# Kernel tuning notes

Measured on AMD Instinct MI355X. Metric: run time of the kernel, lower is better.

The kernel has to match this reference:

```python
import jax, jax.numpy as jnp
import numpy as np

H = 128  # hidden size
I = 19   # input size


def _uniform(key, shape, bound):
    return jax.random.uniform(key, shape, dtype=jnp.float32, minval=-bound, maxval=bound)


def setup_inputs() -> dict:
    key = jax.random.key(0)
    ks = jax.random.split(key, 9)
    bound = 1.0 / np.sqrt(H)  # torch nn.RNN init: U(-1/sqrt(H), 1/sqrt(H))
    x = jax.random.normal(ks[0], (256, 1024, I), dtype=jnp.float32)
    return {
        "x": x,
        "W_ih0": _uniform(ks[1], (H, I), bound),
        "W_hh0": _uniform(ks[2], (H, H), bound),
        "b_ih0": _uniform(ks[3], (H,), bound),
        "b_hh0": _uniform(ks[4], (H,), bound),
        "W_ih1": _uniform(ks[5], (H, H), bound),
        "W_hh1": _uniform(ks[6], (H, H), bound),
        "b_ih1": _uniform(ks[7], (H,), bound),
        "b_hh1": _uniform(ks[8], (H,), bound),
    }


def _rnn_layer(inp, W_ih, W_hh, b_ih, b_hh):
    # inp: [B, T, F]. Precompute input projection for all timesteps (one big GEMM),
    # then scan only the recurrent part: h_t = tanh(pre_t + h_{t-1} @ W_hh^T).
    pre = jnp.einsum('btf,hf->bth', inp, W_ih) + b_ih + b_hh  # [B, T, H]
    h0 = jnp.zeros((inp.shape[0], H), dtype=inp.dtype)

    def step(h, p_t):
        h = jnp.tanh(p_t + h @ W_hh.T)
        return h, h

    _, ys = jax.lax.scan(step, h0, jnp.swapaxes(pre, 0, 1))  # ys: [T, B, H]
    return jnp.swapaxes(ys, 0, 1)  # [B, T, H]


def reference(x, W_ih0, W_hh0, b_ih0, b_hh0, W_ih1, W_hh1, b_ih1, b_hh1):
    out1 = _rnn_layer(x, W_ih0, W_hh0, b_ih0, b_hh0)
    out2 = _rnn_layer(out1, W_ih1, W_hh1, b_ih1, b_hh1)
    return out2
```

## Files before the change

kernel.cpp:

```cpp
#include <hip/hip_runtime.h>
#include <math.h>

#define BATCH 256
#define T 1024
#define IN 19
#define H 128

__device__ __forceinline__ float fast_tanh(float x) {
    float ax = fabsf(x);
    float e  = __expf(2.0f * ax);
    float r  = 1.0f - 2.0f / (e + 1.0f);
    return copysignf(r, x);
}

template <int CTRL>
__device__ __forceinline__ float dppf(float v) {
    return __int_as_float(__builtin_amdgcn_update_dpp(
        0, __float_as_int(v), CTRL, 0xF, 0xF, true));
}
#define XOR1 0xB1
#define XOR2 0x4E
#define XOR8 0x128

__device__ __forceinline__ int uoff(int u) { return (u >> 4) * 20 + (u & 15); }

__global__ __launch_bounds__(512, 2)
void fused_rnn(const float* __restrict__ x,
               const float* __restrict__ Wih0,
               const float* __restrict__ Whh0,
               const float* __restrict__ bih0,
               const float* __restrict__ bhh0,
               const float* __restrict__ Wih1,
               const float* __restrict__ Whh1,
               const float* __restrict__ bih1,
               const float* __restrict__ bhh1,
               float* __restrict__ out) {
    const int b   = blockIdx.x;
    const int tid = threadIdx.x;

    __shared__ __align__(16) float h0ring[4][160];
    __shared__ __align__(16) float h1ring[4][160];
    __shared__ __align__(16) float Bring[4][H];
    __shared__ __align__(16) float xbuf[2][8 * 20];

    if (tid < 128) {
        __builtin_amdgcn_s_setprio(1);
        const bool b0 = tid & 1, b1 = tid & 2, b2 = tid & 8;
        const int s    = (tid & 3) | ((tid & 8) >> 1);
        const int G    = (tid >> 4) * 2 + ((tid >> 2) & 1);
        const int ub   = G * 8;
        const int ufin = ub + (b0 ? 4 : 0) + (b1 ? 2 : 0) + (b2 ? 1 : 0);

        float wA[8][16];
#pragma unroll
        for (int u = 0; u < 8; ++u) {
            const float* wr = Whh0 + (size_t)(ub + u) * H + s * 16;
#pragma unroll
            for (int c = 0; c < 16; c += 4) {
                float4 v = *(const float4*)&wr[c];
                wA[u][c] = v.x; wA[u][c+1] = v.y; wA[u][c+2] = v.z; wA[u][c+3] = v.w;
            }
        }
        float wI[20];
#pragma unroll
        for (int f = 0; f < IN; ++f) wI[f] = Wih0[ufin * IN + f];
        wI[19] = 0.0f;
        const float bias0 = bih0[ufin] + bhh0[ufin];

        const float* xsrc = x + (size_t)b * T * IN;
        const int idx0  = tid;
        const int idx1  = tid + 128;
        const bool v1   = (idx1 < 8 * IN);
        const int slot0 = (idx0 / IN) * 20 + idx0 % IN;
        const int slot1 = (idx1 / IN) * 20 + idx1 % IN;

        if (tid < 8) { xbuf[0][tid * 20 + 19] = 0.0f; xbuf[1][tid * 20 + 19] = 0.0f; }
        xbuf[0][slot0] = xsrc[idx0];
        if (v1) xbuf[0][slot1] = xsrc[idx1];
        float xr0 = xsrc[8 * IN + idx0];
        float xr1 = v1 ? xsrc[8 * IN + idx1] : 0.0f;

        h0ring[3][uoff(ufin)] = 0.0f;
        __syncthreads();

        const int so = s * 20;
        const int wo = uoff(ufin);
        for (int ko = 0; ko < T; ko += 8) {
            const int cb = (ko >> 3) & 1;
            const float* xch = xbuf[cb];
#pragma unroll
            for (int j = 0; j < 8; ++j) {
                const float* xp = &xch[j * 20];
                float4 xv0 = *(const float4*)&xp[0];
                float4 xv1 = *(const float4*)&xp[4];
                float4 xv2 = *(const float4*)&xp[8];
                float4 xv3 = *(const float4*)&xp[12];
                float4 xv4 = *(const float4*)&xp[16];
                float p0 = bias0, p1 = 0.0f;
                p0 = fmaf(xv0.x, wI[0],  p0); p1 = fmaf(xv0.y, wI[1],  p1);
                p0 = fmaf(xv0.z, wI[2],  p0); p1 = fmaf(xv0.w, wI[3],  p1);
                p0 = fmaf(xv1.x, wI[4],  p0); p1 = fmaf(xv1.y, wI[5],  p1);
                p0 = fmaf(xv1.z, wI[6],  p0); p1 = fmaf(xv1.w, wI[7],  p1);
                p0 = fmaf(xv2.x, wI[8],  p0); p1 = fmaf(xv2.y, wI[9],  p1);
                p0 = fmaf(xv2.z, wI[10], p0); p1 = fmaf(xv2.w, wI[11], p1);
                p0 = fmaf(xv3.x, wI[12], p0); p1 = fmaf(xv3.y, wI[13], p1);
                p0 = fmaf(xv3.z, wI[14], p0); p1 = fmaf(xv3.w, wI[15], p1);
                p0 = fmaf(xv4.x, wI[16], p0); p1 = fmaf(xv4.y, wI[17], p1);
                p0 = fmaf(xv4.z, wI[18], p0); p1 = fmaf(xv4.w, wI[19], p1);
                const float* hp = &h0ring[(j + 3) & 3][so];
                float d0=0,d1=0,d2=0,d3=0,d4=0,d5=0,d6=0,d7=0;
#pragma unroll
                for (int c = 0; c < 16; c += 4) {
                    float4 hv = *(const float4*)&hp[c];
                    d0 = fmaf(wA[0][c],hv.x,d0); d0 = fmaf(wA[0][c+1],hv.y,d0); d0 = fmaf(wA[0][c+2],hv.z,d0); d0 = fmaf(wA[0][c+3],hv.w,d0);
                    d1 = fmaf(wA[1][c],hv.x,d1); d1 = fmaf(wA[1][c+1],hv.y,d1); d1 = fmaf(wA[1][c+2],hv.z,d1); d1 = fmaf(wA[1][c+3],hv.w,d1);
                    d2 = fmaf(wA[2][c],hv.x,d2); d2 = fmaf(wA[2][c+1],hv.y,d2); d2 = fmaf(wA[2][c+2],hv.z,d2); d2 = fmaf(wA[2][c+3],hv.w,d2);
                    d3 = fmaf(wA[3][c],hv.x,d3); d3 = fmaf(wA[3][c+1],hv.y,d3); d3 = fmaf(wA[3][c+2],hv.z,d3); d3 = fmaf(wA[3][c+3],hv.w,d3);
                    d4 = fmaf(wA[4][c],hv.x,d4); d4 = fmaf(wA[4][c+1],hv.y,d4); d4 = fmaf(wA[4][c+2],hv.z,d4); d4 = fmaf(wA[4][c+3],hv.w,d4);
                    d5 = fmaf(wA[5][c],hv.x,d5); d5 = fmaf(wA[5][c+1],hv.y,d5); d5 = fmaf(wA[5][c+2],hv.z,d5); d5 = fmaf(wA[5][c+3],hv.w,d5);
                    d6 = fmaf(wA[6][c],hv.x,d6); d6 = fmaf(wA[6][c+1],hv.y,d6); d6 = fmaf(wA[6][c+2],hv.z,d6); d6 = fmaf(wA[6][c+3],hv.w,d6);
                    d7 = fmaf(wA[7][c],hv.x,d7); d7 = fmaf(wA[7][c+1],hv.y,d7); d7 = fmaf(wA[7][c+2],hv.z,d7); d7 = fmaf(wA[7][c+3],hv.w,d7);
                }
                float e0 = (b0 ? d4 : d0) + dppf<XOR1>(b0 ? d0 : d4);
                float e1 = (b0 ? d5 : d1) + dppf<XOR1>(b0 ? d1 : d5);
                float e2 = (b0 ? d6 : d2) + dppf<XOR1>(b0 ? d2 : d6);
                float e3 = (b0 ? d7 : d3) + dppf<XOR1>(b0 ? d3 : d7);
                float g0 = (b1 ? e2 : e0) + dppf<XOR2>(b1 ? e0 : e2);
                float g1 = (b1 ? e3 : e1) + dppf<XOR2>(b1 ? e1 : e3);
                float f  = (b2 ? g1 : g0) + dppf<XOR8>(b2 ? g0 : g1);
                h0ring[j & 3][wo] = fast_tanh(f + p0 + p1);
                if (j == 7) {
                    if (ko + 8 < T) {
                        float* xd = xbuf[cb ^ 1];
                        xd[slot0] = xr0;
                        if (v1) xd[slot1] = xr1;
                    }
                    if (ko + 16 < T) {
                        const float* xs2 = xsrc + (size_t)(ko + 16) * IN;
                        xr0 = xs2[idx0];
                        if (v1) xr1 = xs2[idx1];
                    }
                }
                __syncthreads();
            }
        }
        __syncthreads();
        __syncthreads();
    } else if (tid < 384) {
        const int p  = tid - 128;
        const bool b0 = p & 1, b1 = p & 2;
        const int s    = (p & 3) | ((p & 8) >> 1);
        const int Gp   = (p >> 4) * 2 + ((p >> 2) & 1);
        const int ub   = Gp * 4;
        const int ufin = ub + (b0 ? 2 : 0) + (b1 ? 1 : 0);

        float wP[4][16];
#pragma unroll
        for (int u = 0; u < 4; ++u) {
            const float* wr = Wih1 + (size_t)(ub + u) * H + s * 16;
#pragma unroll
            for (int c = 0; c < 16; c += 4) {
                float4 v = *(const float4*)&wr[c];
                wP[u][c] = v.x; wP[u][c+1] = v.y; wP[u][c+2] = v.z; wP[u][c+3] = v.w;
            }
        }
        const float biasP = bih1[ufin] + bhh1[ufin];

        __syncthreads();
        __syncthreads();

        const int so = s * 20;
        for (int ko = 1; ko < 1025; ko += 8) {
#pragma unroll
            for (int j = 0; j < 8; ++j) {
                const float* hp = &h0ring[j & 3][so];
                float d0=0,d1=0,d2=0,d3=0;
#pragma unroll
                for (int c = 0; c < 16; c += 4) {
                    float4 hv = *(const float4*)&hp[c];
                    d0 = fmaf(wP[0][c],hv.x,d0); d0 = fmaf(wP[0][c+1],hv.y,d0); d0 = fmaf(wP[0][c+2],hv.z,d0); d0 = fmaf(wP[0][c+3],hv.w,d0);
                    d1 = fmaf(wP[1][c],hv.x,d1); d1 = fmaf(wP[1][c+1],hv.y,d1); d1 = fmaf(wP[1][c+2],hv.z,d1); d1 = fmaf(wP[1][c+3],hv.w,d1);
                    d2 = fmaf(wP[2][c],hv.x,d2); d2 = fmaf(wP[2][c+1],hv.y,d2); d2 = fmaf(wP[2][c+2],hv.z,d2); d2 = fmaf(wP[2][c+3],hv.w,d2);
                    d3 = fmaf(wP[3][c],hv.x,d3); d3 = fmaf(wP[3][c+1],hv.y,d3); d3 = fmaf(wP[3][c+2],hv.z,d3); d3 = fmaf(wP[3][c+3],hv.w,d3);
                }
                float e0 = (b0 ? d2 : d0) + dppf<XOR1>(b0 ? d0 : d2);
                float e1 = (b0 ? d3 : d1) + dppf<XOR1>(b0 ? d1 : d3);
                float g  = (b1 ? e1 : e0) + dppf<XOR2>(b1 ? e0 : e1);
                g += dppf<XOR8>(g);
                if (!(p & 8)) Bring[j & 3][ufin] = g + biasP;
                __syncthreads();
            }
        }
        __syncthreads();
    } else {
        __builtin_amdgcn_s_setprio(1);
        const int w  = tid - 384;
        const bool b0 = w & 1, b1 = w & 2, b2 = w & 8;
        const int s    = (w & 3) | ((w & 8) >> 1);
        const int G    = (w >> 4) * 2 + ((w >> 2) & 1);
        const int ub   = G * 8;
        const int ufin = ub + (b0 ? 4 : 0) + (b1 ? 2 : 0) + (b2 ? 1 : 0);

        float wA[8][16];
#pragma unroll
        for (int u = 0; u < 8; ++u) {
            const float* wr = Whh1 + (size_t)(ub + u) * H + s * 16;
#pragma unroll
            for (int c = 0; c < 16; c += 4) {
                float4 v = *(const float4*)&wr[c];
                wA[u][c] = v.x; wA[u][c+1] = v.y; wA[u][c+2] = v.z; wA[u][c+3] = v.w;
            }
        }
        float* orow = out + (size_t)b * T * H + ufin;
        float sbuf[8];

        h1ring[3][uoff(ufin)] = 0.0f;
        __syncthreads();
        __syncthreads();
        __syncthreads();

        const int so = s * 20;
        const int wo = uoff(ufin);
        for (int ko = 2; ko < 1026; ko += 8) {
#pragma unroll
            for (int j = 0; j < 8; ++j) {
                const float* hp = &h1ring[(j + 3) & 3][so];
                float Bg = Bring[j & 3][ufin];
                float d0=0,d1=0,d2=0,d3=0,d4=0,d5=0,d6=0,d7=0;
#pragma unroll
                for (int c = 0; c < 16; c += 4) {
                    float4 hv = *(const float4*)&hp[c];
                    d0 = fmaf(wA[0][c],hv.x,d0); d0 = fmaf(wA[0][c+1],hv.y,d0); d0 = fmaf(wA[0][c+2],hv.z,d0); d0 = fmaf(wA[0][c+3],hv.w,d0);
                    d1 = fmaf(wA[1][c],hv.x,d1); d1 = fmaf(wA[1][c+1],hv.y,d1); d1 = fmaf(wA[1][c+2],hv.z,d1); d1 = fmaf(wA[1][c+3],hv.w,d1);
                    d2 = fmaf(wA[2][c],hv.x,d2); d2 = fmaf(wA[2][c+1],hv.y,d2); d2 = fmaf(wA[2][c+2],hv.z,d2); d2 = fmaf(wA[2][c+3],hv.w,d2);
                    d3 = fmaf(wA[3][c],hv.x,d3); d3 = fmaf(wA[3][c+1],hv.y,d3); d3 = fmaf(wA[3][c+2],hv.z,d3); d3 = fmaf(wA[3][c+3],hv.w,d3);
                    d4 = fmaf(wA[4][c],hv.x,d4); d4 = fmaf(wA[4][c+1],hv.y,d4); d4 = fmaf(wA[4][c+2],hv.z,d4); d4 = fmaf(wA[4][c+3],hv.w,d4);
                    d5 = fmaf(wA[5][c],hv.x,d5); d5 = fmaf(wA[5][c+1],hv.y,d5); d5 = fmaf(wA[5][c+2],hv.z,d5); d5 = fmaf(wA[5][c+3],hv.w,d5);
                    d6 = fmaf(wA[6][c],hv.x,d6); d6 = fmaf(wA[6][c+1],hv.y,d6); d6 = fmaf(wA[6][c+2],hv.z,d6); d6 = fmaf(wA[6][c+3],hv.w,d6);
                    d7 = fmaf(wA[7][c],hv.x,d7); d7 = fmaf(wA[7][c+1],hv.y,d7); d7 = fmaf(wA[7][c+2],hv.z,d7); d7 = fmaf(wA[7][c+3],hv.w,d7);
                }
                float e0 = (b0 ? d4 : d0) + dppf<XOR1>(b0 ? d0 : d4);
                float e1 = (b0 ? d5 : d1) + dppf<XOR1>(b0 ? d1 : d5);
                float e2 = (b0 ? d6 : d2) + dppf<XOR1>(b0 ? d2 : d6);
                float e3 = (b0 ? d7 : d3) + dppf<XOR1>(b0 ? d3 : d7);
                float g0 = (b1 ? e2 : e0) + dppf<XOR2>(b1 ? e0 : e2);
                float g1 = (b1 ? e3 : e1) + dppf<XOR2>(b1 ? e1 : e3);
                float f  = (b2 ? g1 : g0) + dppf<XOR8>(b2 ? g0 : g1);
                float h1v = fast_tanh(Bg + f);
                h1ring[j & 3][wo] = h1v;
                sbuf[j] = h1v;
                if (j == 7) {
                    const int t0 = ko - 2;
#pragma unroll
                    for (int i = 0; i < 8; ++i)
                        orow[(size_t)(t0 + i) * H] = sbuf[i];
                }
                __syncthreads();
            }
        }
    }
}

extern "C" void kernel_launch(void* const* d_in, const int* in_sizes, int n_in,
                              void* d_out, int out_size, void* d_ws, size_t ws_size,
                              hipStream_t stream) {
    const float* x     = (const float*)d_in[0];
    const float* W_ih0 = (const float*)d_in[1];
    const float* W_hh0 = (const float*)d_in[2];
    const float* b_ih0 = (const float*)d_in[3];
    const float* b_hh0 = (const float*)d_in[4];
    const float* W_ih1 = (const float*)d_in[5];
    const float* W_hh1 = (const float*)d_in[6];
    const float* b_ih1 = (const float*)d_in[7];
    const float* b_hh1 = (const float*)d_in[8];

    float* out = (float*)d_out;

    fused_rnn<<<BATCH, 512, 0, stream>>>(x, W_ih0, W_hh0, b_ih0, b_hh0,
                                         W_ih1, W_hh1, b_ih1, b_hh1, out);
}
```

Baseline: 658.7 us.

## Move layer-0 input projection to middle warps and use lightweight barriers

The layer-0 input projection and x staging move out of the critical recurrent warp into the layer-1 projection warps. Those warps compute the next timestep's projection into a new shared ring buffer one step ahead, and the layer-1 pipeline stage is shifted to match. All __syncthreads calls are replaced with a custom barrier that waits only on LDS counters, not global memory. This shortens the serial layer-0 step, at the cost of more work on the middle warps and subtler memory-ordering assumptions around the barrier.

```diff
diff --git a/kernel.cpp b/kernel.cpp
--- a/kernel.cpp
+++ b/kernel.cpp
@@ -21,6 +21,12 @@
 #define XOR1 0xB1
 #define XOR2 0x4E
 #define XOR8 0x128
+
+__device__ __forceinline__ void sync_fast() {
+    asm volatile("s_waitcnt lgkmcnt(0)" ::: "memory");
+    __builtin_amdgcn_s_barrier();
+    asm volatile("" ::: "memory");
+}
 
 __device__ __forceinline__ int uoff(int u) { return (u >> 4) * 20 + (u & 15); }
 
@@ -41,6 +47,7 @@
     __shared__ __align__(16) float h0ring[4][160];
     __shared__ __align__(16) float h1ring[4][160];
     __shared__ __align__(16) float Bring[4][H];
+    __shared__ __align__(16) float projring[4][H];
     __shared__ __align__(16) float xbuf[2][8 * 20];
 
     if (tid < 128) {
@@ -61,53 +68,24 @@
                 wA[u][c] = v.x; wA[u][c+1] = v.y; wA[u][c+2] = v.z; wA[u][c+3] = v.w;
             }
         }
-        float wI[20];
-#pragma unroll
-        for (int f = 0; f < IN; ++f) wI[f] = Wih0[ufin * IN + f];
-        wI[19] = 0.0f;
-        const float bias0 = bih0[ufin] + bhh0[ufin];
-
-        const float* xsrc = x + (size_t)b * T * IN;
-        const int idx0  = tid;
-        const int idx1  = tid + 128;
-        const bool v1   = (idx1 < 8 * IN);
-        const int slot0 = (idx0 / IN) * 20 + idx0 % IN;
-        const int slot1 = (idx1 / IN) * 20 + idx1 % IN;
-
-        if (tid < 8) { xbuf[0][tid * 20 + 19] = 0.0f; xbuf[1][tid * 20 + 19] = 0.0f; }
-        xbuf[0][slot0] = xsrc[idx0];
-        if (v1) xbuf[0][slot1] = xsrc[idx1];
-        float xr0 = xsrc[8 * IN + idx0];
-        float xr1 = v1 ? xsrc[8 * IN + idx1] : 0.0f;
-
+        {
+            const float* wr = Wih0 + ufin * IN;
+            const float* xr = x + (size_t)b * T * IN;
+            float acc = bih0[ufin] + bhh0[ufin];
+#pragma unroll
+            for (int f = 0; f < IN; ++f) acc = fmaf(xr[f], wr[f], acc);
+            projring[0][ufin] = acc;
+        }
         h0ring[3][uoff(ufin)] = 0.0f;
-        __syncthreads();
+        sync_fast();
 
         const int so = s * 20;
         const int wo = uoff(ufin);
         for (int ko = 0; ko < T; ko += 8) {
-            const int cb = (ko >> 3) & 1;
-            const float* xch = xbuf[cb];
 #pragma unroll
             for (int j = 0; j < 8; ++j) {
-                const float* xp = &xch[j * 20];
-                float4 xv0 = *(const float4*)&xp[0];
-                float4 xv1 = *(const float4*)&xp[4];
-                float4 xv2 = *(const float4*)&xp[8];
-                float4 xv3 = *(const float4*)&xp[12];
-                float4 xv4 = *(const float4*)&xp[16];
-                float p0 = bias0, p1 = 0.0f;
-                p0 = fmaf(xv0.x, wI[0],  p0); p1 = fmaf(xv0.y, wI[1],  p1);
-                p0 = fmaf(xv0.z, wI[2],  p0); p1 = fmaf(xv0.w, wI[3],  p1);
-                p0 = fmaf(xv1.x, wI[4],  p0); p1 = fmaf(xv1.y, wI[5],  p1);
-                p0 = fmaf(xv1.z, wI[6],  p0); p1 = fmaf(xv1.w, wI[7],  p1);
-                p0 = fmaf(xv2.x, wI[8],  p0); p1 = fmaf(xv2.y, wI[9],  p1);
-                p0 = fmaf(xv2.z, wI[10], p0); p1 = fmaf(xv2.w, wI[11], p1);
-                p0 = fmaf(xv3.x, wI[12], p0); p1 = fmaf(xv3.y, wI[13], p1);
-                p0 = fmaf(xv3.z, wI[14], p0); p1 = fmaf(xv3.w, wI[15], p1);
-                p0 = fmaf(xv4.x, wI[16], p0); p1 = fmaf(xv4.y, wI[17], p1);
-                p0 = fmaf(xv4.z, wI[18], p0); p1 = fmaf(xv4.w, wI[19], p1);
                 const float* hp = &h0ring[(j + 3) & 3][so];
+                float pcur = projring[j & 3][ufin];
                 float d0=0,d1=0,d2=0,d3=0,d4=0,d5=0,d6=0,d7=0;
 #pragma unroll
                 for (int c = 0; c < 16; c += 4) {
@@ -128,24 +106,12 @@
                 float g0 = (b1 ? e2 : e0) + dppf<XOR2>(b1 ? e0 : e2);
                 float g1 = (b1 ? e3 : e1) + dppf<XOR2>(b1 ? e1 : e3);
                 float f  = (b2 ? g1 : g0) + dppf<XOR8>(b2 ? g0 : g1);
-                h0ring[j & 3][wo] = fast_tanh(f + p0 + p1);
-                if (j == 7) {
-                    if (ko + 8 < T) {
-                        float* xd = xbuf[cb ^ 1];
-                        xd[slot0] = xr0;
-                        if (v1) xd[slot1] = xr1;
-                    }
-                    if (ko + 16 < T) {
-                        const float* xs2 = xsrc + (size_t)(ko + 16) * IN;
-                        xr0 = xs2[idx0];
-                        if (v1) xr1 = xs2[idx1];
-                    }
-                }
-                __syncthreads();
-            }
-        }
-        __syncthreads();
-        __syncthreads();
+                h0ring[j & 3][wo] = fast_tanh(pcur + f);
+                sync_fast();
+            }
+        }
+        sync_fast();
+        sync_fast();
     } else if (tid < 384) {
         const int p  = tid - 128;
         const bool b0 = p & 1, b1 = p & 2;
@@ -166,14 +132,39 @@
         }
         const float biasP = bih1[ufin] + bhh1[ufin];
 
-        __syncthreads();
-        __syncthreads();
+        const bool hasProj = (p >= 128);
+        const int pu = p - 128;
+        float wIP[20];
+        float biasPr = 0.0f;
+        const float* xsrc = x + (size_t)b * T * IN + IN;
+        const int idx0  = pu;
+        const int idx1  = pu + 128;
+        const bool v1   = hasProj && (pu < 24);
+        const int slot0 = hasProj ? ((idx0 / IN) * 20 + idx0 % IN) : 0;
+        const int slot1 = hasProj ? ((idx1 / IN) * 20 + idx1 % IN) : 0;
+        const int XMAX  = (T - 1) * IN - 1;
+        float xr0 = 0.0f, xr1 = 0.0f;
+
+        if (hasProj) {
+            const float* wr = Wih0 + (size_t)pu * IN;
+#pragma unroll
+            for (int f = 0; f < IN; ++f) wIP[f] = wr[f];
+            wIP[19] = 0.0f;
+            biasPr = bih0[pu] + bhh0[pu];
+            if (pu < 8) { xbuf[0][pu * 20 + 19] = 0.0f; xbuf[1][pu * 20 + 19] = 0.0f; }
+            xbuf[0][slot0] = xsrc[idx0];
+            if (v1) xbuf[0][slot1] = xsrc[idx1];
+            xr0 = xsrc[152 + idx0];
+            if (v1) xr1 = xsrc[152 + idx1];
+        }
+        sync_fast();
 
         const int so = s * 20;
-        for (int ko = 1; ko < 1025; ko += 8) {
+        for (int ko = 0; ko < T; ko += 8) {
+            const int cb = (ko >> 3) & 1;
 #pragma unroll
             for (int j = 0; j < 8; ++j) {
-                const float* hp = &h0ring[j & 3][so];
+                const float* hp = &h0ring[(j + 3) & 3][so];
                 float d0=0,d1=0,d2=0,d3=0;
 #pragma unroll
                 for (int c = 0; c < 16; c += 4) {
@@ -187,11 +178,59 @@
                 float e1 = (b0 ? d3 : d1) + dppf<XOR1>(b0 ? d1 : d3);
                 float g  = (b1 ? e1 : e0) + dppf<XOR2>(b1 ? e0 : e1);
                 g += dppf<XOR8>(g);
-                if (!(p & 8)) Bring[j & 3][ufin] = g + biasP;
-                __syncthreads();
-            }
-        }
-        __syncthreads();
+                if (!(p & 8)) Bring[(j + 3) & 3][ufin] = g + biasP;
+                if (hasProj) {
+                    const float* xp = &xbuf[cb][j * 20];
+                    float4 xv0 = *(const float4*)&xp[0];
+                    float4 xv1 = *(const float4*)&xp[4];
+                    float4 xv2 = *(const float4*)&xp[8];
+                    float4 xv3 = *(const float4*)&xp[12];
+                    float4 xv4 = *(const float4*)&xp[16];
+                    float p0 = biasPr, p1 = 0.0f;
+                    p0 = fmaf(xv0.x, wIP[0],  p0); p1 = fmaf(xv0.y, wIP[1],  p1);
+                    p0 = fmaf(xv0.z, wIP[2],  p0); p1 = fmaf(xv0.w, wIP[3],  p1);
+                    p0 = fmaf(xv1.x, wIP[4],  p0); p1 = fmaf(xv1.y, wIP[5],  p1);
+                    p0 = fmaf(xv1.z, wIP[6],  p0); p1 = fmaf(xv1.w, wIP[7],  p1);
+                    p0 = fmaf(xv2.x, wIP[8],  p0); p1 = fmaf(xv2.y, wIP[9],  p1);
+                    p0 = fmaf(xv2.z, wIP[10], p0); p1 = fmaf(xv2.w, wIP[11], p1);
+                    p0 = fmaf(xv3.x, wIP[12], p0); p1 = fmaf(xv3.y, wIP[13], p1);
+                    p0 = fmaf(xv3.z, wIP[14], p0); p1 = fmaf(xv3.w, wIP[15], p1);
+                    p0 = fmaf(xv4.x, wIP[16], p0); p1 = fmaf(xv4.y, wIP[17], p1);
+                    p0 = fmaf(xv4.z, wIP[18], p0); p1 = fmaf(xv4.w, wIP[19], p1);
+                    projring[(j + 1) & 3][pu] = p0 + p1;
+                    if (j == 7) {
+                        float* xd = xbuf[cb ^ 1];
+                        xd[slot0] = xr0;
+                        if (v1) xd[slot1] = xr1;
+                        const int c2 = (ko >> 3) + 2;
+                        int o0 = 152 * c2 + idx0; o0 = o0 > XMAX ? XMAX : o0;
+                        int o1 = 152 * c2 + idx1; o1 = o1 > XMAX ? XMAX : o1;
+                        xr0 = xsrc[o0];
+                        if (v1) xr1 = xsrc[o1];
+                    }
+                }
+                sync_fast();
+            }
+        }
+        {
+            const float* hp = &h0ring[3][so];
+            float d0=0,d1=0,d2=0,d3=0;
+#pragma unroll
+            for (int c = 0; c < 16; c += 4) {
+                float4 hv = *(const float4*)&hp[c];
+                d0 = fmaf(wP[0][c],hv.x,d0); d0 = fmaf(wP[0][c+1],hv.y,d0); d0 = fmaf(wP[0][c+2],hv.z,d0); d0 = fmaf(wP[0][c+3],hv.w,d0);
+                d1 = fmaf(wP[1][c],hv.x,d1); d1 = fmaf(wP[1][c+1],hv.y,d1); d1 = fmaf(wP[1][c+2],hv.z,d1); d1 = fmaf(wP[1][c+3],hv.w,d1);
+                d2 = fmaf(wP[2][c],hv.x,d2); d2 = fmaf(wP[2][c+1],hv.y,d2); d2 = fmaf(wP[2][c+2],hv.z,d2); d2 = fmaf(wP[2][c+3],hv.w,d2);
+                d3 = fmaf(wP[3][c],hv.x,d3); d3 = fmaf(wP[3][c+1],hv.y,d3); d3 = fmaf(wP[3][c+2],hv.z,d3); d3 = fmaf(wP[3][c+3],hv.w,d3);
+            }
+            float e0 = (b0 ? d2 : d0) + dppf<XOR1>(b0 ? d0 : d2);
+            float e1 = (b0 ? d3 : d1) + dppf<XOR1>(b0 ? d1 : d3);
+            float g  = (b1 ? e1 : e0) + dppf<XOR2>(b1 ? e0 : e1);
+            g += dppf<XOR8>(g);
+            if (!(p & 8)) Bring[3][ufin] = g + biasP;
+        }
+        sync_fast();
+        sync_fast();
     } else {
         __builtin_amdgcn_s_setprio(1);
         const int w  = tid - 384;
@@ -215,9 +254,9 @@
         float sbuf[8];
 
         h1ring[3][uoff(ufin)] = 0.0f;
-        __syncthreads();
-        __syncthreads();
-        __syncthreads();
+        sync_fast();
+        sync_fast();
+        sync_fast();
 
         const int so = s * 20;
         const int wo = uoff(ufin);
@@ -255,7 +294,7 @@
                     for (int i = 0; i < 8; ++i)
                         orow[(size_t)(t0 + i) * H] = sbuf[i];
                 }
-                __syncthreads();
+                sync_fast();
             }
         }
     }
```

Result: faster. 608.7 us (-7.6%).

## Replace block barriers with per-wave LDS flag dataflow pipeline across RNN stages

Applied to the files above, without the earlier changes.

Replaces the per-timestep __syncthreads lockstep with per-wave progress counters in shared memory that each stage spins on, so layer-0 recurrence, layer-1 input projection, layer-0 input projection and layer-1 recurrence can run decoupled through 8-deep ring buffers. The layer-0 input projection moves from the recurrence waves into a dedicated pair of waves, which removes it from the critical serial path. The layer-1 projection is rebalanced to 8 units per thread. Spin-waiting with s_sleep and waitcnt fences adds polling cost and relies on LDS ordering between waves, and a spin cap could silently break correctness if a wait ever exceeds it.

```diff
diff --git a/kernel.cpp b/kernel.cpp
--- a/kernel.cpp
+++ b/kernel.cpp
@@ -22,9 +22,14 @@
 #define XOR2 0x4E
 #define XOR8 0x128
 
+#define FENCE asm volatile("" ::: "memory")
+#define LGKM0 asm volatile("s_waitcnt lgkmcnt(0)" ::: "memory")
+#define MAXSPIN (1 << 22)
+
 __device__ __forceinline__ int uoff(int u) { return (u >> 4) * 20 + (u & 15); }
 
-__global__ __launch_bounds__(512, 2)
+__global__ __launch_bounds__(512)
+__attribute__((amdgpu_waves_per_eu(2, 2)))
 void fused_rnn(const float* __restrict__ x,
                const float* __restrict__ Wih0,
                const float* __restrict__ Whh0,
@@ -38,18 +43,30 @@
     const int b   = blockIdx.x;
     const int tid = threadIdx.x;
 
-    __shared__ __align__(16) float h0ring[4][160];
-    __shared__ __align__(16) float h1ring[4][160];
-    __shared__ __align__(16) float Bring[4][H];
-    __shared__ __align__(16) float xbuf[2][8 * 20];
-
+    __shared__ __align__(16) float h0ring[8][160];
+    __shared__ __align__(16) float h1ring[8][160];
+    __shared__ __align__(16) float Bring[8][H];
+    __shared__ __align__(16) float projring[8][H];
+    __shared__ __align__(8)  int  flags[8];
+    volatile int* vf = (volatile int*)flags;
+
+    if (tid < 8) flags[tid] = 0;
     if (tid < 128) {
+        h0ring[7][uoff(tid)] = 0.0f;
+        h1ring[7][uoff(tid)] = 0.0f;
+    }
+    __syncthreads();
+
+    const int wave = tid >> 6;
+
+    if (wave < 2) {
         __builtin_amdgcn_s_setprio(1);
         const bool b0 = tid & 1, b1 = tid & 2, b2 = tid & 8;
         const int s    = (tid & 3) | ((tid & 8) >> 1);
         const int G    = (tid >> 4) * 2 + ((tid >> 2) & 1);
         const int ub   = G * 8;
         const int ufin = ub + (b0 ? 4 : 0) + (b1 ? 2 : 0) + (b2 ? 1 : 0);
+        const int myf  = wave;
 
         float wA[8][16];
 #pragma unroll
@@ -61,53 +78,26 @@
                 wA[u][c] = v.x; wA[u][c+1] = v.y; wA[u][c+2] = v.z; wA[u][c+3] = v.w;
             }
         }
-        float wI[20];
-#pragma unroll
-        for (int f = 0; f < IN; ++f) wI[f] = Wih0[ufin * IN + f];
-        wI[19] = 0.0f;
-        const float bias0 = bih0[ufin] + bhh0[ufin];
-
-        const float* xsrc = x + (size_t)b * T * IN;
-        const int idx0  = tid;
-        const int idx1  = tid + 128;
-        const bool v1   = (idx1 < 8 * IN);
-        const int slot0 = (idx0 / IN) * 20 + idx0 % IN;
-        const int slot1 = (idx1 / IN) * 20 + idx1 % IN;
-
-        if (tid < 8) { xbuf[0][tid * 20 + 19] = 0.0f; xbuf[1][tid * 20 + 19] = 0.0f; }
-        xbuf[0][slot0] = xsrc[idx0];
-        if (v1) xbuf[0][slot1] = xsrc[idx1];
-        float xr0 = xsrc[8 * IN + idx0];
-        float xr1 = v1 ? xsrc[8 * IN + idx1] : 0.0f;
-
-        h0ring[3][uoff(ufin)] = 0.0f;
-        __syncthreads();
-
         const int so = s * 20;
         const int wo = uoff(ufin);
+
         for (int ko = 0; ko < T; ko += 8) {
-            const int cb = (ko >> 3) & 1;
-            const float* xch = xbuf[cb];
 #pragma unroll
             for (int j = 0; j < 8; ++j) {
-                const float* xp = &xch[j * 20];
-                float4 xv0 = *(const float4*)&xp[0];
-                float4 xv1 = *(const float4*)&xp[4];
-                float4 xv2 = *(const float4*)&xp[8];
-                float4 xv3 = *(const float4*)&xp[12];
-                float4 xv4 = *(const float4*)&xp[16];
-                float p0 = bias0, p1 = 0.0f;
-                p0 = fmaf(xv0.x, wI[0],  p0); p1 = fmaf(xv0.y, wI[1],  p1);
-                p0 = fmaf(xv0.z, wI[2],  p0); p1 = fmaf(xv0.w, wI[3],  p1);
-                p0 = fmaf(xv1.x, wI[4],  p0); p1 = fmaf(xv1.y, wI[5],  p1);
-                p0 = fmaf(xv1.z, wI[6],  p0); p1 = fmaf(xv1.w, wI[7],  p1);
-                p0 = fmaf(xv2.x, wI[8],  p0); p1 = fmaf(xv2.y, wI[9],  p1);
-                p0 = fmaf(xv2.z, wI[10], p0); p1 = fmaf(xv2.w, wI[11], p1);
-                p0 = fmaf(xv3.x, wI[12], p0); p1 = fmaf(xv3.y, wI[13], p1);
-                p0 = fmaf(xv3.z, wI[14], p0); p1 = fmaf(xv3.w, wI[15], p1);
-                p0 = fmaf(xv4.x, wI[16], p0); p1 = fmaf(xv4.y, wI[17], p1);
-                p0 = fmaf(xv4.z, wI[18], p0); p1 = fmaf(xv4.w, wI[19], p1);
-                const float* hp = &h0ring[(j + 3) & 3][so];
+                const int k = ko + j;
+                {
+                    const int np = k + 1, nh = k, nb = k - 7;
+                    for (int it = 0; ; ++it) {
+                        if (vf[4] >= np && vf[5] >= np &&
+                            vf[0] >= nh && vf[1] >= nh &&
+                            vf[2] >= nb && vf[3] >= nb) break;
+                        if (it >= MAXSPIN) break;
+                        __builtin_amdgcn_s_sleep(1);
+                    }
+                    FENCE;
+                }
+                float pcur = projring[j][ufin];
+                const float* hp = &h0ring[(j + 7) & 7][so];
                 float d0=0,d1=0,d2=0,d3=0,d4=0,d5=0,d6=0,d7=0;
 #pragma unroll
                 for (int c = 0; c < 16; c += 4) {
@@ -128,78 +118,120 @@
                 float g0 = (b1 ? e2 : e0) + dppf<XOR2>(b1 ? e0 : e2);
                 float g1 = (b1 ? e3 : e1) + dppf<XOR2>(b1 ? e1 : e3);
                 float f  = (b2 ? g1 : g0) + dppf<XOR8>(b2 ? g0 : g1);
-                h0ring[j & 3][wo] = fast_tanh(f + p0 + p1);
-                if (j == 7) {
-                    if (ko + 8 < T) {
-                        float* xd = xbuf[cb ^ 1];
-                        xd[slot0] = xr0;
-                        if (v1) xd[slot1] = xr1;
-                    }
-                    if (ko + 16 < T) {
-                        const float* xs2 = xsrc + (size_t)(ko + 16) * IN;
-                        xr0 = xs2[idx0];
-                        if (v1) xr1 = xs2[idx1];
-                    }
-                }
-                __syncthreads();
-            }
-        }
-        __syncthreads();
-        __syncthreads();
-    } else if (tid < 384) {
+                h0ring[j][wo] = fast_tanh(pcur + f);
+                LGKM0;
+                vf[myf] = k + 1;
+                FENCE;
+            }
+        }
+    } else if (wave < 4) {
         const int p  = tid - 128;
-        const bool b0 = p & 1, b1 = p & 2;
+        const bool b0 = p & 1, b1 = p & 2, b2 = p & 8;
         const int s    = (p & 3) | ((p & 8) >> 1);
-        const int Gp   = (p >> 4) * 2 + ((p >> 2) & 1);
-        const int ub   = Gp * 4;
-        const int ufin = ub + (b0 ? 2 : 0) + (b1 ? 1 : 0);
-
-        float wP[4][16];
-#pragma unroll
-        for (int u = 0; u < 4; ++u) {
+        const int G    = (p >> 4) * 2 + ((p >> 2) & 1);
+        const int ub   = G * 8;
+        const int ufin = ub + (b0 ? 4 : 0) + (b1 ? 2 : 0) + (b2 ? 1 : 0);
+        const int myf  = 2 + (wave - 2);
+
+        float wB[8][16];
+#pragma unroll
+        for (int u = 0; u < 8; ++u) {
             const float* wr = Wih1 + (size_t)(ub + u) * H + s * 16;
 #pragma unroll
             for (int c = 0; c < 16; c += 4) {
                 float4 v = *(const float4*)&wr[c];
-                wP[u][c] = v.x; wP[u][c+1] = v.y; wP[u][c+2] = v.z; wP[u][c+3] = v.w;
+                wB[u][c] = v.x; wB[u][c+1] = v.y; wB[u][c+2] = v.z; wB[u][c+3] = v.w;
             }
         }
         const float biasP = bih1[ufin] + bhh1[ufin];
-
-        __syncthreads();
-        __syncthreads();
-
         const int so = s * 20;
-        for (int ko = 1; ko < 1025; ko += 8) {
+
+        for (int ko = 0; ko < T; ko += 8) {
 #pragma unroll
             for (int j = 0; j < 8; ++j) {
-                const float* hp = &h0ring[j & 3][so];
-                float d0=0,d1=0,d2=0,d3=0;
+                const int k = ko + j;
+                {
+                    const int nh = k + 1, nl = k - 7;
+                    for (int it = 0; ; ++it) {
+                        if (vf[0] >= nh && vf[1] >= nh &&
+                            vf[6] >= nl && vf[7] >= nl) break;
+                        if (it >= MAXSPIN) break;
+                        __builtin_amdgcn_s_sleep(1);
+                    }
+                    FENCE;
+                }
+                const float* hp = &h0ring[j][so];
+                float d0=0,d1=0,d2=0,d3=0,d4=0,d5=0,d6=0,d7=0;
 #pragma unroll
                 for (int c = 0; c < 16; c += 4) {
                     float4 hv = *(const float4*)&hp[c];
-                    d0 = fmaf(wP[0][c],hv.x,d0); d0 = fmaf(wP[0][c+1],hv.y,d0); d0 = fmaf(wP[0][c+2],hv.z,d0); d0 = fmaf(wP[0][c+3],hv.w,d0);
-                    d1 = fmaf(wP[1][c],hv.x,d1); d1 = fmaf(wP[1][c+1],hv.y,d1); d1 = fmaf(wP[1][c+2],hv.z,d1); d1 = fmaf(wP[1][c+3],hv.w,d1);
-                    d2 = fmaf(wP[2][c],hv.x,d2); d2 = fmaf(wP[2][c+1],hv.y,d2); d2 = fmaf(wP[2][c+2],hv.z,d2); d2 = fmaf(wP[2][c+3],hv.w,d2);
-                    d3 = fmaf(wP[3][c],hv.x,d3); d3 = fmaf(wP[3][c+1],hv.y,d3); d3 = fmaf(wP[3][c+2],hv.z,d3); d3 = fmaf(wP[3][c+3],hv.w,d3);
-                }
-                float e0 = (b0 ? d2 : d0) + dppf<XOR1>(b0 ? d0 : d2);
-                float e1 = (b0 ? d3 : d1) + dppf<XOR1>(b0 ? d1 : d3);
-                float g  = (b1 ? e1 : e0) + dppf<XOR2>(b1 ? e0 : e1);
-                g += dppf<XOR8>(g);
-                if (!(p & 8)) Bring[j & 3][ufin] = g + biasP;
-                __syncthreads();
-            }
-        }
-        __syncthreads();
+                    d0 = fmaf(wB[0][c],hv.x,d0); d0 = fmaf(wB[0][c+1],hv.y,d0); d0 = fmaf(wB[0][c+2],hv.z,d0); d0 = fmaf(wB[0][c+3],hv.w,d0);
+                    d1 = fmaf(wB[1][c],hv.x,d1); d1 = fmaf(wB[1][c+1],hv.y,d1); d1 = fmaf(wB[1][c+2],hv.z,d1); d1 = fmaf(wB[1][c+3],hv.w,d1);
+                    d2 = fmaf(wB[2][c],hv.x,d2); d2 = fmaf(wB[2][c+1],hv.y,d2); d2 = fmaf(wB[2][c+2],hv.z,d2); d2 = fmaf(wB[2][c+3],hv.w,d2);
+                    d3 = fmaf(wB[3][c],hv.x,d3); d3 = fmaf(wB[3][c+1],hv.y,d3); d3 = fmaf(wB[3][c+2],hv.z,d3); d3 = fmaf(wB[3][c+3],hv.w,d3);
+                    d4 = fmaf(wB[4][c],hv.x,d4); d4 = fmaf(wB[4][c+1],hv.y,d4); d4 = fmaf(wB[4][c+2],hv.z,d4); d4 = fmaf(wB[4][c+3],hv.w,d4);
+                    d5 = fmaf(wB[5][c],hv.x,d5); d5 = fmaf(wB[5][c+1],hv.y,d5); d5 = fmaf(wB[5][c+2],hv.z,d5); d5 = fmaf(wB[5][c+3],hv.w,d5);
+                    d6 = fmaf(wB[6][c],hv.x,d6); d6 = fmaf(wB[6][c+1],hv.y,d6); d6 = fmaf(wB[6][c+2],hv.z,d6); d6 = fmaf(wB[6][c+3],hv.w,d6);
+                    d7 = fmaf(wB[7][c],hv.x,d7); d7 = fmaf(wB[7][c+1],hv.y,d7); d7 = fmaf(wB[7][c+2],hv.z,d7); d7 = fmaf(wB[7][c+3],hv.w,d7);
+                }
+                float e0 = (b0 ? d4 : d0) + dppf<XOR1>(b0 ? d0 : d4);
+                float e1 = (b0 ? d5 : d1) + dppf<XOR1>(b0 ? d1 : d5);
+                float e2 = (b0 ? d6 : d2) + dppf<XOR1>(b0 ? d2 : d6);
+                float e3 = (b0 ? d7 : d3) + dppf<XOR1>(b0 ? d3 : d7);
+                float g0 = (b1 ? e2 : e0) + dppf<XOR2>(b1 ? e0 : e2);
+                float g1 = (b1 ? e3 : e1) + dppf<XOR2>(b1 ? e1 : e3);
+                float f  = (b2 ? g1 : g0) + dppf<XOR8>(b2 ? g0 : g1);
+                Bring[j][ufin] = f + biasP;
+                LGKM0;
+                vf[myf] = k + 1;
+                FENCE;
+            }
+        }
+    } else if (wave < 6) {
+        const int q   = tid - 256;
+        const int myf = 4 + (wave - 4);
+
+        float wI[IN];
+        {
+            const float* wr = Wih0 + (size_t)q * IN;
+#pragma unroll
+            for (int f = 0; f < IN; ++f) wI[f] = wr[f];
+        }
+        const float bias0 = bih0[q] + bhh0[q];
+        const float* xb = x + (size_t)b * T * IN;
+
+        for (int ko = 0; ko < T; ko += 8) {
+#pragma unroll
+            for (int j = 0; j < 8; ++j) {
+                const int k = ko + j;
+                {
+                    const int nl = k - 7;
+                    for (int it = 0; ; ++it) {
+                        if (vf[0] >= nl && vf[1] >= nl) break;
+                        if (it >= MAXSPIN) break;
+                        __builtin_amdgcn_s_sleep(1);
+                    }
+                    FENCE;
+                }
+                const float* xr = xb + (size_t)k * IN;
+                float acc = bias0;
+#pragma unroll
+                for (int f = 0; f < IN; ++f) acc = fmaf(xr[f], wI[f], acc);
+                projring[j][q] = acc;
+                LGKM0;
+                vf[myf] = k + 1;
+                FENCE;
+            }
+        }
     } else {
         __builtin_amdgcn_s_setprio(1);
-        const int w  = tid - 384;
-        const bool b0 = w & 1, b1 = w & 2, b2 = w & 8;
-        const int s    = (w & 3) | ((w & 8) >> 1);
-        const int G    = (w >> 4) * 2 + ((w >> 2) & 1);
+        const int r  = tid - 384;
+        const bool b0 = r & 1, b1 = r & 2, b2 = r & 8;
+        const int s    = (r & 3) | ((r & 8) >> 1);
+        const int G    = (r >> 4) * 2 + ((r >> 2) & 1);
         const int ub   = G * 8;
         const int ufin = ub + (b0 ? 4 : 0) + (b1 ? 2 : 0) + (b2 ? 1 : 0);
+        const int myf  = 6 + (wave - 6);
 
         float wA[8][16];
 #pragma unroll
@@ -212,20 +244,25 @@
             }
         }
         float* orow = out + (size_t)b * T * H + ufin;
-        float sbuf[8];
-
-        h1ring[3][uoff(ufin)] = 0.0f;
-        __syncthreads();
-        __syncthreads();
-        __syncthreads();
-
         const int so = s * 20;
         const int wo = uoff(ufin);
-        for (int ko = 2; ko < 1026; ko += 8) {
+
+        for (int ko = 0; ko < T; ko += 8) {
 #pragma unroll
             for (int j = 0; j < 8; ++j) {
-                const float* hp = &h1ring[(j + 3) & 3][so];
-                float Bg = Bring[j & 3][ufin];
+                const int t = ko + j;
+                {
+                    const int nb = t + 1, nh = t;
+                    for (int it = 0; ; ++it) {
+                        if (vf[2] >= nb && vf[3] >= nb &&
+                            vf[6] >= nh && vf[7] >= nh) break;
+                        if (it >= MAXSPIN) break;
+                        __builtin_amdgcn_s_sleep(1);
+                    }
+                    FENCE;
+                }
+                float Bg = Bring[j][ufin];
+                const float* hp = &h1ring[(j + 7) & 7][so];
                 float d0=0,d1=0,d2=0,d3=0,d4=0,d5=0,d6=0,d7=0;
 #pragma unroll
                 for (int c = 0; c < 16; c += 4) {
@@ -247,15 +284,11 @@
                 float g1 = (b1 ? e3 : e1) + dppf<XOR2>(b1 ? e1 : e3);
                 float f  = (b2 ? g1 : g0) + dppf<XOR8>(b2 ? g0 : g1);
                 float h1v = fast_tanh(Bg + f);
-                h1ring[j & 3][wo] = h1v;
-                sbuf[j] = h1v;
-                if (j == 7) {
-                    const int t0 = ko - 2;
-#pragma unroll
-                    for (int i = 0; i < 8; ++i)
-                        orow[(size_t)(t0 + i) * H] = sbuf[i];
-                }
-                __syncthreads();
+                h1ring[j][wo] = h1v;
+                LGKM0;
+                vf[myf] = t + 1;
+                FENCE;
+                orow[(size_t)t * H] = h1v;
             }
         }
     }
```

Measured after the change: 933.4 us. 41.7% more time.
